# Kernel optimization log

Measured on AMD Instinct MI355X. Metric: run time of the kernel, lower is better.

Reference implementation:

```python
import jax, jax.numpy as jnp
import numpy as np

H_BLK, K_BLK = 2, 2      # h = out_ch//64, k = in_ch//64
HOS = 64                 # hyper_out_size
NR = 8                   # num_radii of hypernet-generated filters
KS = 3                   # kernel size
SD, HD = 6, 128          # seidel_dim, hyper_dim
CIN, COUT = K_BLK * HOS, H_BLK * HOS
B, HH, WW = 2, 256, 256
BN_EPS = 1e-5


def setup_inputs() -> dict:
    key = jax.random.key(0)
    ks = jax.random.split(key, 16)
    rn = lambda k, shape, s=1.0: jax.random.normal(k, shape, dtype=jnp.float32) * s
    n1, n2 = H_BLK * K_BLK, H_BLK * H_BLK
    hyper_out = HOS * HOS * NR * KS * KS  # 294912
    return {
        "x": rn(ks[0], (B, CIN, HH, WW)),
        "seidel": rn(ks[1], (B, SD)),
        "m1_w1": rn(ks[2], (n1, SD, HD), 1.0 / np.sqrt(SD)),
        "m1_b1": rn(ks[3], (n1, HD), 0.01),
        "m1_w2": rn(ks[4], (n1, HD, HD), 1.0 / np.sqrt(HD)),
        "m1_b2": rn(ks[5], (n1, HD), 0.01),
        "m2_w1": rn(ks[6], (n2, SD, HD), 1.0 / np.sqrt(SD)),
        "m2_b1": rn(ks[7], (n2, HD), 0.01),
        "m2_w2": rn(ks[8], (n2, HD, HD), 1.0 / np.sqrt(HD)),
        "m2_b2": rn(ks[9], (n2, HD), 0.01),
        "hyper_w": rn(ks[10], (HD, hyper_out), 0.02),
        "hyper_b": rn(ks[11], (hyper_out,), 0.01),
        "bn1_gamma": jnp.ones((COUT,), jnp.float32),
        "bn1_beta": jnp.zeros((COUT,), jnp.float32),
        "bn2_gamma": jnp.ones((COUT,), jnp.float32),
        "bn2_beta": jnp.zeros((COUT,), jnp.float32),
    }


def _gen_weights(s, mw1, mb1, mw2, mb2, hyper_w, hyper_b, rows, cols):
    # s: [SD]; one MLP per (row, col) block, hypernet shared.
    e = jax.nn.relu(jnp.einsum('i,nio->no', s, mw1) + mb1)       # [n, HD]
    e = jax.nn.relu(jnp.einsum('ni,nio->no', e, mw2) + mb2)      # [n, HD] (dropout = eval identity)
    blk = (e @ hyper_w + hyper_b).reshape(rows, cols, HOS, HOS, NR, KS, KS)
    # cat dim=1 over cols (c_in), cat dim=0 over rows (c_out)
    return blk.transpose(0, 2, 1, 3, 4, 5, 6).reshape(rows * HOS, cols * HOS, NR, KS, KS)


def _interp_w(w, wd):
    # trilinear interp (align_corners=False) along radii axis to wd points; k,k axes are identity.
    nr = w.shape[2]
    pos = jnp.clip((jnp.arange(wd, dtype=jnp.float32) + 0.5) * (nr / wd) - 0.5, 0.0, nr - 1.0)
    i0 = jnp.floor(pos).astype(jnp.int32)
    i1 = jnp.minimum(i0 + 1, nr - 1)
    f = (pos - i0.astype(jnp.float32))[None, None, :, None, None]
    return w[:, :, i0] * (1.0 - f) + w[:, :, i1] * f              # [cout, cin, wd, KS, KS]


def _lri_conv(x1, wi):
    # x1: [cin, H, W]; wi: [cout, cin, W, KS, KS]; circular pad in H, zero pad in W.
    c, h, w = x1.shape
    p = 1
    xp = jnp.pad(x1, ((0, 0), (p, p), (0, 0)), mode='wrap')
    xp = jnp.pad(xp, ((0, 0), (0, 0), (p, p)))
    out = jnp.zeros((wi.shape[0], h, w), x1.dtype)
    for ki in range(KS):
        for kj in range(KS):
            out = out + jnp.einsum('ihw,oiw->ohw', xp[:, ki:ki + h, kj:kj + w], wi[:, :, :, ki, kj])
    return out


def _bn_relu(y, g, b):
    # per-item training-mode BN (torch loop feeds one item at a time): stats over H,W per channel
    mu = y.mean(axis=(1, 2), keepdims=True)
    var = y.var(axis=(1, 2), keepdims=True)
    return jax.nn.relu(g[:, None, None] * (y - mu) * jax.lax.rsqrt(var + BN_EPS) + b[:, None, None])


def _forward(x, seidel, m1_w1, m1_b1, m1_w2, m1_b2, m2_w1, m2_b1, m2_w2, m2_b2,
             hyper_w, hyper_b, bn1_gamma, bn1_beta, bn2_gamma, bn2_beta):
    wd = x.shape[-1]

    def per_item(xi, si):
        w1 = _interp_w(_gen_weights(si, m1_w1, m1_b1, m1_w2, m1_b2, hyper_w, hyper_b, H_BLK, K_BLK), wd)
        y = _bn_relu(_lri_conv(xi, w1), bn1_gamma, bn1_beta)
        w2 = _interp_w(_gen_weights(si, m2_w1, m2_b1, m2_w2, m2_b2, hyper_w, hyper_b, H_BLK, H_BLK), wd)
        return _bn_relu(_lri_conv(y, w2), bn2_gamma, bn2_beta)

    return jax.vmap(per_item)(x, seidel)


def reference(x, seidel, m1_w1, m1_b1, m1_w2, m1_b2, m2_w1, m2_b1, m2_w2, m2_b2,
              hyper_w, hyper_b, bn1_gamma, bn1_beta, bn2_gamma, bn2_beta):
    return _forward(x, seidel, m1_w1, m1_b1, m1_w2, m1_b2, m2_w1, m2_b1, m2_w2, m2_b2,
                    hyper_w, hyper_b, bn1_gamma, bn1_beta, bn2_gamma, bn2_beta)
```

## Files before the change

kernel.cpp:

```cpp
#include <hip/hip_runtime.h>
#include <hip/hip_bf16.h>


#define SD 6
#define HD 128
#define HYPER_OUT 294912
#define BN_EPS 1e-5f

typedef unsigned short ushort_t;
typedef __attribute__((ext_vector_type(8))) short bf16x8;
typedef __attribute__((ext_vector_type(4))) float f32x4;

__device__ inline ushort_t f2bf(float f) {
  union { float f; unsigned u; } v; v.f = f;
  unsigned r = v.u + 0x7fffu + ((v.u >> 16) & 1u);
  return (ushort_t)(r >> 16);
}
__device__ inline float bf2f(ushort_t h) {
  union { unsigned u; float f; } v; v.u = ((unsigned)h) << 16; return v.f;
}
__device__ inline unsigned pack2(float a, float b) {
  return (unsigned)f2bf(a) | ((unsigned)f2bf(b) << 16);
}

__device__ inline bf16x8 lerp8d(bf16x8 a, bf16x8 d, float f) {
  union U { bf16x8 v; unsigned u[4]; };
  U A, D, R;
  A.v = a; D.v = d;
  #pragma unroll
  for (int i = 0; i < 4; ++i) {
    float alo = __uint_as_float(A.u[i] << 16);
    float ahi = __uint_as_float(A.u[i] & 0xffff0000u);
    float dlo = __uint_as_float(D.u[i] << 16);
    float dhi = __uint_as_float(D.u[i] & 0xffff0000u);
    float rlo = fmaf(f, dlo, alo);
    float rhi = fmaf(f, dhi, ahi);
    __hip_bfloat162 h2 = __float22bfloat162_rn(float2{rlo, rhi});
    R.u[i] = *reinterpret_cast<unsigned*>(&h2);
  }
  return R.v;
}

__device__ inline int as_off(int row, int cu) {
  return row*128 + ((cu ^ (row & 7)) << 3);
}

__global__ __launch_bounds__(128) void k_mlp(
    const float* __restrict__ seidel,
    const float* __restrict__ m1_w1, const float* __restrict__ m1_b1,
    const float* __restrict__ m1_w2, const float* __restrict__ m1_b2,
    const float* __restrict__ m2_w1, const float* __restrict__ m2_b1,
    const float* __restrict__ m2_w2, const float* __restrict__ m2_b2,
    float* __restrict__ e_all)
{
  int b = blockIdx.x;
  int item = b >> 3, conv = (b >> 2) & 1, n = b & 3;
  const float* w1 = conv ? m2_w1 : m1_w1;
  const float* b1 = conv ? m2_b1 : m1_b1;
  const float* w2 = conv ? m2_w2 : m1_w2;
  const float* b2 = conv ? m2_b2 : m1_b2;
  int t = threadIdx.x;
  __shared__ float e1[HD];
  float s = b1[n*HD + t];
  #pragma unroll
  for (int i = 0; i < SD; ++i) s = fmaf(seidel[item*SD + i], w1[(n*SD + i)*HD + t], s);
  e1[t] = fmaxf(s, 0.f);
  __syncthreads();
  float s2 = b2[n*HD + t];
  for (int i = 0; i < HD; ++i) s2 = fmaf(e1[i], w2[(n*HD + i)*HD + t], s2);
  e_all[b*HD + t] = fmaxf(s2, 0.f);
}

__global__ __launch_bounds__(256) void k_hyper(
    const float* __restrict__ e_all, const float* __restrict__ hyper_w,
    const float* __restrict__ hyper_b, ushort_t* __restrict__ wb_lin)
{
  __shared__ float es[16*HD];
  int t = threadIdx.x;
  for (int f = t; f < 16*HD; f += 256) es[f] = e_all[f];
  __syncthreads();
  int j = blockIdx.x*256 + t;
  float val[16];
  #pragma unroll
  for (int r = 0; r < 16; ++r) val[r] = 0.f;
  for (int i = 0; i < HD; ++i) {
    float hw = hyper_w[(size_t)i*HYPER_OUT + j];
    #pragma unroll
    for (int r = 0; r < 16; ++r) val[r] = fmaf(es[r*HD + i], hw, val[r]);
  }
  float bias = hyper_b[j];
  uint4 u0, u1;
  u0.x = pack2(val[0]+bias,  val[1]+bias);
  u0.y = pack2(val[2]+bias,  val[3]+bias);
  u0.z = pack2(val[4]+bias,  val[5]+bias);
  u0.w = pack2(val[6]+bias,  val[7]+bias);
  u1.x = pack2(val[8]+bias,  val[9]+bias);
  u1.y = pack2(val[10]+bias, val[11]+bias);
  u1.z = pack2(val[12]+bias, val[13]+bias);
  u1.w = pack2(val[14]+bias, val[15]+bias);
  *reinterpret_cast<uint4*>(wb_lin + (size_t)j*16)     = u0;
  *reinterpret_cast<uint4*>(wb_lin + (size_t)j*16 + 8) = u1;
}

__global__ __launch_bounds__(256) void k_prep(
    const float* __restrict__ x, ushort_t* __restrict__ xt,
    const ushort_t* __restrict__ wb_lin,
    ushort_t* __restrict__ wbW, ushort_t* __restrict__ wbD)
{
  __shared__ __align__(16) float tileF[64][65];
  __shared__ ushort_t ldsN[16][256];
  int b = blockIdx.x;
  int t = threadIdx.x;
  if (b < 4096) {
    int wt = b & 3, ct = (b >> 2) & 1, z = b >> 3;
    int h = z & 255, item = z >> 8;
    {
      int cl = t >> 2, wk = (t & 3) << 4;
      const float* sp = x + (((size_t)item*128 + ct*64 + cl)*256 + h)*256 + wt*64 + wk;
      #pragma unroll
      for (int k = 0; k < 16; k += 4) {
        float4 v = *reinterpret_cast<const float4*>(sp + k);
        tileF[cl][wk+k] = v.x; tileF[cl][wk+k+1] = v.y;
        tileF[cl][wk+k+2] = v.z; tileF[cl][wk+k+3] = v.w;
      }
    }
    __syncthreads();
    {
      int wl = t >> 2, ck = (t & 3) << 4;
      ushort_t* dp = xt + (((size_t)item*256 + wt*64 + wl)*256 + h)*128 + ct*64 + ck;
      uint4 u0, u1;
      u0.x = pack2(tileF[ck+0][wl],  tileF[ck+1][wl]);
      u0.y = pack2(tileF[ck+2][wl],  tileF[ck+3][wl]);
      u0.z = pack2(tileF[ck+4][wl],  tileF[ck+5][wl]);
      u0.w = pack2(tileF[ck+6][wl],  tileF[ck+7][wl]);
      u1.x = pack2(tileF[ck+8][wl],  tileF[ck+9][wl]);
      u1.y = pack2(tileF[ck+10][wl], tileF[ck+11][wl]);
      u1.z = pack2(tileF[ck+12][wl], tileF[ck+13][wl]);
      u1.w = pack2(tileF[ck+14][wl], tileF[ck+15][wl]);
      *reinterpret_cast<uint4*>(dp)     = u0;
      *reinterpret_cast<uint4*>(dp + 8) = u1;
    }
  } else {
    int i = b - 4096;
    int chunk = i & 15;
    int tap   = i >> 4;
    int nr = tap / 9, kk = tap % 9;
    int ki = kk / 3, kj = kk % 3;
    int nrn = (nr < 7) ? nr + 1 : 7;
    ushort_t (*lds)[256] = reinterpret_cast<ushort_t(*)[256]>(tileF);
    int uv = chunk*256 + t;
    size_t j  = (size_t)uv*72 + nr*9 + kk;
    size_t j2 = (size_t)uv*72 + nrn*9 + kk;
    uint4 q0 = *reinterpret_cast<const uint4*>(wb_lin + j*16);
    uint4 q1 = *reinterpret_cast<const uint4*>(wb_lin + j*16 + 8);
    uint4 n0 = *reinterpret_cast<const uint4*>(wb_lin + j2*16);
    uint4 n1 = *reinterpret_cast<const uint4*>(wb_lin + j2*16 + 8);
    const ushort_t* pr0 = reinterpret_cast<const ushort_t*>(&q0);
    const ushort_t* pr1 = reinterpret_cast<const ushort_t*>(&q1);
    const ushort_t* pn0 = reinterpret_cast<const ushort_t*>(&n0);
    const ushort_t* pn1 = reinterpret_cast<const ushort_t*>(&n1);
    #pragma unroll
    for (int r = 0; r < 8; ++r) { lds[r][t]  = pr0[r]; ldsN[r][t]  = pn0[r]; }
    #pragma unroll
    for (int r = 0; r < 8; ++r) { lds[r+8][t] = pr1[r]; ldsN[r+8][t] = pn1[r]; }
    __syncthreads();
    #pragma unroll
    for (int it = 0; it < 2; ++it) {
      int idx = it*256 + t;
      int row = idx >> 3, seg = idx & 7;
      int p = row >> 2, ul = row & 3;
      int item = p >> 3, conv = (p >> 2) & 1, n = p & 3;
      int o  = (n >> 1)*64 + chunk*4 + ul;
      int c8 = (n & 1)*8 + seg;
      int ch = c8 >> 2, gq = c8 & 3;
      int oblk = o >> 4, ol = o & 15;
      uint4 v = *reinterpret_cast<const uint4*>(&lds[p][ul*64 + seg*8]);
      uint4 d4;
      {
        const ushort_t* pw = reinterpret_cast<const ushort_t*>(&v);
        const ushort_t* pnx = &ldsN[p][ul*64 + seg*8];
        ushort_t* pd = reinterpret_cast<ushort_t*>(&d4);
        #pragma unroll
        for (int e = 0; e < 8; ++e) pd[e] = f2bf(bf2f(pnx[e]) - bf2f(pw[e]));
      }
      size_t off = (size_t)(conv*2 + item)*1179648
                 + ((((size_t)nr*3 + kj)*3 + ki)*4 + ch)*4096
                 + oblk*512 + (gq*16 + ol)*8;
      *reinterpret_cast<uint4*>(wbW + off) = v;
      *reinterpret_cast<uint4*>(wbD + off) = d4;
    }
  }
}

template<bool BN_IN>
__global__ __launch_bounds__(256, 2) void k_conv(
    const ushort_t* __restrict__ src,
    const ushort_t* __restrict__ wbW, const ushort_t* __restrict__ wbD,
    const float* __restrict__ bn_a, const float* __restrict__ bn_c,
    ushort_t* __restrict__ dst, float* __restrict__ ps, float* __restrict__ p2)
{
  __shared__ __align__(16) ushort_t As[258*128];
  __shared__ float sbn[256];
  int bid = blockIdx.x;
  int wgid = ((bid & 7) << 6) | (bid >> 3);
  int item = wgid >> 8;
  int w    = wgid & 255;
  int t = threadIdx.x;
  int lane = t & 63, wid = t >> 6;
  int l15 = lane & 15, g = lane >> 4;

  float pos = fminf(fmaxf((w + 0.5f)*0.03125f - 0.5f, 0.f), 7.f);
  int i0 = (int)pos; float fr = pos - (float)i0;

  if constexpr (BN_IN) {
    sbn[t] = (t < 128) ? bn_a[item*128 + t] : bn_c[item*128 + (t - 128)];
    __syncthreads();
  }

  const ushort_t* wpW = wbW + (size_t)item*1179648 + (size_t)i0*147456
                      + (wid*2)*512 + lane*8;
  const ushort_t* wpD = wbD + (size_t)item*1179648 + (size_t)i0*147456
                      + (wid*2)*512 + lane*8;

  f32x4 acc[2][16];
  #pragma unroll
  for (int a = 0; a < 2; ++a)
    #pragma unroll
    for (int b = 0; b < 16; ++b)
      acc[a][b] = (f32x4){0.f, 0.f, 0.f, 0.f};

  auto stage_as = [&](int kj) {
    int wc = w + kj - 1;
    bool valid = (wc >= 0) && (wc < 256);
    const ushort_t* sb = src + ((size_t)item*256 + (valid ? wc : 0))*32768;
    for (int f = t; f < 258*16; f += 256) {
      int row = f >> 4, cu = f & 15;
      uint4 v = make_uint4(0u, 0u, 0u, 0u);
      if (valid) {
        int hg = (row + 255) & 255;
        v = *reinterpret_cast<const uint4*>(sb + ((size_t)hg << 7) + (cu << 3));
        if constexpr (BN_IN) {
          ushort_t* pv = reinterpret_cast<ushort_t*>(&v);
          int c0 = cu << 3;
          #pragma unroll
          for (int jj = 0; jj < 8; ++jj) {
            float xv = bf2f(pv[jj]);
            xv = fmaxf(fmaf(sbn[c0 + jj], xv, sbn[128 + c0 + jj]), 0.f);
            pv[jj] = f2bf(xv);
          }
        }
      }
      *reinterpret_cast<uint4*>(&As[as_off(row, cu)]) = v;
    }
  };

  auto loadraw = [&](bf16x8* rw, bf16x8* rd, int s) {
    size_t so = (size_t)s*4096;
    #pragma unroll
    for (int mf = 0; mf < 2; ++mf) {
      rw[mf] = *reinterpret_cast<const bf16x8*>(wpW + so + mf*512);
      rd[mf] = *reinterpret_cast<const bf16x8*>(wpD + so + mf*512);
    }
  };

  bf16x8 rwA[2], rdA[2], rwB[2], rdB[2], lw[2];
  loadraw(rwA, rdA, 0);

  for (int kj = 0; kj < 3; ++kj) {
    __syncthreads();
    stage_as(kj);
    __syncthreads();
    #pragma unroll
    for (int s2 = 0; s2 < 12; ++s2) {
      int ki = s2 >> 2, ch = s2 & 3;
      int s = kj*12 + s2;
      bf16x8* cw = (s2 & 1) ? rwB : rwA;
      bf16x8* cd = (s2 & 1) ? rdB : rdA;
      bf16x8* nw = (s2 & 1) ? rwA : rwB;
      bf16x8* nd = (s2 & 1) ? rdA : rdB;
      loadraw(nw, nd, (s + 1 < 36) ? (s + 1) : 35);
      #pragma unroll
      for (int mf = 0; mf < 2; ++mf) lw[mf] = lerp8d(cw[mf], cd[mf], fr);
      #pragma unroll
      for (int pass = 0; pass < 4; ++pass) {
        bf16x8 bfr[4];
        #pragma unroll
        for (int q = 0; q < 4; ++q) {
          int nf = pass*4 + q;
          bfr[q] = *reinterpret_cast<const bf16x8*>(
              &As[as_off(nf*16 + l15 + ki, (ch << 2) + g)]);
        }
        #pragma unroll
        for (int mf = 0; mf < 2; ++mf)
          #pragma unroll
          for (int q = 0; q < 4; ++q)
            acc[mf][pass*4 + q] = __builtin_amdgcn_mfma_f32_16x16x32_bf16(
                lw[mf], bfr[q], acc[mf][pass*4 + q], 0, 0, 0);
      }
    }
  }

  ushort_t* yb = dst + ((size_t)item*256 + w)*32768;
  float ssum[2][4], s2sum[2][4];
  #pragma unroll
  for (int a = 0; a < 2; ++a)
    #pragma unroll
    for (int b = 0; b < 4; ++b) { ssum[a][b] = 0.f; s2sum[a][b] = 0.f; }
  #pragma unroll
  for (int mf = 0; mf < 2; ++mf) {
    #pragma unroll
    for (int nf = 0; nf < 16; ++nf) {
      float v[4];
      #pragma unroll
      for (int r4 = 0; r4 < 4; ++r4) {
        v[r4] = acc[mf][nf][r4];
        ssum[mf][r4] += v[r4];
        s2sum[mf][r4] = fmaf(v[r4], v[r4], s2sum[mf][r4]);
      }
      int h  = nf*16 + l15;
      int o0 = wid*32 + mf*16 + (g << 2);
      uint2 u; u.x = pack2(v[0], v[1]); u.y = pack2(v[2], v[3]);
      *reinterpret_cast<uint2*>(yb + (size_t)h*128 + o0) = u;
    }
  }
  #pragma unroll
  for (int mf = 0; mf < 2; ++mf)
    #pragma unroll
    for (int r4 = 0; r4 < 4; ++r4)
      #pragma unroll
      for (int m = 1; m < 16; m <<= 1) {
        ssum[mf][r4]  += __shfl_xor(ssum[mf][r4], m);
        s2sum[mf][r4] += __shfl_xor(s2sum[mf][r4], m);
      }
  __syncthreads();
  float* redS  = reinterpret_cast<float*>(As);
  float* redS2 = redS + 128;
  if (l15 == 0) {
    #pragma unroll
    for (int mf = 0; mf < 2; ++mf)
      #pragma unroll
      for (int r4 = 0; r4 < 4; ++r4) {
        int o = wid*32 + mf*16 + (g << 2) + r4;
        redS [o] = ssum[mf][r4];
        redS2[o] = s2sum[mf][r4];
      }
  }
  __syncthreads();
  if (t < 128) {
    size_t bi = (size_t)item*256 + w;
    ps[bi*128 + t] = redS[t];
    p2[bi*128 + t] = redS2[t];
  }
}

__global__ __launch_bounds__(256) void k_bnapply(
    const float* __restrict__ ps, const float* __restrict__ p2,
    const float* __restrict__ gamma, const float* __restrict__ beta,
    float* __restrict__ bn_a, float* __restrict__ bn_c)
{
  int item = blockIdx.x >> 7, o = blockIdx.x & 127;
  int t = threadIdx.x;
  size_t bi = (size_t)(item*256 + t)*128 + o;
  float s  = ps[bi];
  float s2 = p2[bi];
  #pragma unroll
  for (int m = 1; m < 64; m <<= 1) { s += __shfl_xor(s, m); s2 += __shfl_xor(s2, m); }
  __shared__ float rs[4], rs2[4];
  if ((t & 63) == 0) { rs[t >> 6] = s; rs2[t >> 6] = s2; }
  __syncthreads();
  if (t == 0) {
    s  = rs[0] + rs[1] + rs[2] + rs[3];
    s2 = rs2[0] + rs2[1] + rs2[2] + rs2[3];
    float mu  = s  * (1.f/65536.f);
    float var = s2 * (1.f/65536.f) - mu*mu;
    float a = gamma[o] * rsqrtf(var + BN_EPS);
    bn_a[item*128 + o] = a;
    bn_c[item*128 + o] = beta[o] - a*mu;
  }
}

__global__ __launch_bounds__(256) void k_final(
    const ushort_t* __restrict__ y, const float* __restrict__ bn_a,
    const float* __restrict__ bn_c, float* __restrict__ out)
{
  __shared__ float tile[64][65];
  int wt = blockIdx.x, ot = blockIdx.y;
  int h = blockIdx.z & 255, item = blockIdx.z >> 8;
  int t = threadIdx.x;
  {
    int wl = t >> 2, ck = (t & 3) << 4;
    const ushort_t* sp = y + (((size_t)item*256 + wt*64 + wl)*256 + h)*128 + ot*64 + ck;
    uint4 a = *reinterpret_cast<const uint4*>(sp);
    uint4 b = *reinterpret_cast<const uint4*>(sp + 8);
    const ushort_t* pa = reinterpret_cast<const ushort_t*>(&a);
    const ushort_t* pb = reinterpret_cast<const ushort_t*>(&b);
    #pragma unroll
    for (int k = 0; k < 8; ++k) {
      int o = ot*64 + ck + k;
      tile[wl][ck + k] = fmaxf(fmaf(bn_a[item*128 + o], bf2f(pa[k]), bn_c[item*128 + o]), 0.f);
    }
    #pragma unroll
    for (int k = 0; k < 8; ++k) {
      int o = ot*64 + ck + 8 + k;
      tile[wl][ck + 8 + k] = fmaxf(fmaf(bn_a[item*128 + o], bf2f(pb[k]), bn_c[item*128 + o]), 0.f);
    }
  }
  __syncthreads();
  {
    int ol = t >> 2, wk = (t & 3) << 4;
    float* dp = out + (((size_t)item*128 + ot*64 + ol)*256 + h)*256 + wt*64 + wk;
    #pragma unroll
    for (int k = 0; k < 16; k += 4) {
      float4 v;
      v.x = tile[wk+k][ol];   v.y = tile[wk+k+1][ol];
      v.z = tile[wk+k+2][ol]; v.w = tile[wk+k+3][ol];
      *reinterpret_cast<float4*>(dp + k) = v;
    }
  }
}

extern "C" void kernel_launch(void* const* d_in, const int* in_sizes, int n_in,
                              void* d_out, int out_size, void* d_ws, size_t ws_size,
                              hipStream_t stream) {
  const float* x       = (const float*)d_in[0];
  const float* seidel  = (const float*)d_in[1];
  const float* m1_w1   = (const float*)d_in[2];
  const float* m1_b1   = (const float*)d_in[3];
  const float* m1_w2   = (const float*)d_in[4];
  const float* m1_b2   = (const float*)d_in[5];
  const float* m2_w1   = (const float*)d_in[6];
  const float* m2_b1   = (const float*)d_in[7];
  const float* m2_w2   = (const float*)d_in[8];
  const float* m2_b2   = (const float*)d_in[9];
  const float* hyper_w = (const float*)d_in[10];
  const float* hyper_b = (const float*)d_in[11];
  const float* bn1_g   = (const float*)d_in[12];
  const float* bn1_b   = (const float*)d_in[13];
  const float* bn2_g   = (const float*)d_in[14];
  const float* bn2_b   = (const float*)d_in[15];

  char* ws = (char*)d_ws;
  float*    e_all  = (float*)ws;
  ushort_t* wb_lin = (ushort_t*)(ws + 8192);
  ushort_t* wbW    = (ushort_t*)(ws + 9445376);
  ushort_t* wbD    = (ushort_t*)(ws + 18882560);
  ushort_t* xt     = (ushort_t*)(ws + 28319744);
  ushort_t* y1     = (ushort_t*)(ws + 61874176);
  ushort_t* y2     = (ushort_t*)(ws + 95428608);
  float*    ps     = (float*)(ws + 128983040);
  float*    p2     = (float*)(ws + 129245184);
  float*    bnb    = (float*)(ws + 129507328);
  float* bn1_a = bnb,        *bn1_c = bnb + 256;
  float* bn2_a = bnb + 512,  *bn2_c = bnb + 768;

  k_mlp<<<16, 128, 0, stream>>>(seidel, m1_w1, m1_b1, m1_w2, m1_b2,
                                m2_w1, m2_b1, m2_w2, m2_b2, e_all);
  k_hyper<<<HYPER_OUT/256, 256, 0, stream>>>(e_all, hyper_w, hyper_b, wb_lin);
  k_prep<<<5248, 256, 0, stream>>>(x, xt, wb_lin, wbW, wbD);

  k_conv<false><<<512, 256, 0, stream>>>(xt, wbW, wbD, nullptr, nullptr, y1, ps, p2);
  k_bnapply<<<256, 256, 0, stream>>>(ps, p2, bn1_g, bn1_b, bn1_a, bn1_c);

  k_conv<true><<<512, 256, 0, stream>>>(y1, wbW + 2359296, wbD + 2359296,
                                        bn1_a, bn1_c, y2, ps, p2);
  k_bnapply<<<256, 256, 0, stream>>>(ps, p2, bn2_g, bn2_b, bn2_a, bn2_c);
  k_final<<<dim3(4, 2, 512), 256, 0, stream>>>(y2, bn2_a, bn2_c, (float*)d_out);
}
```

Measured before the change: 256.9 us.

## Switch conv inner product to 32x32x16 MFMA with matching weight layout

The conv kernel moves from 16x16x32 bf16 MFMA tiles (2x16 fragments per wave) to 32x32x16 tiles (8 fragments of 32 outputs by 32 rows). The weight pre-pack kernel is rewritten to emit the matching per-lane layout. Each K-slice now needs one weight fragment and one lerp per lane instead of two, and each A-fragment LDS read feeds a larger MFMA. This is meant to cut LDS traffic and lerp work per FLOP. In exchange there are twice as many K steps, and the reduction shuffles and the epilogue output mapping change.

```diff
diff --git a/kernel.cpp b/kernel.cpp
--- a/kernel.cpp
+++ b/kernel.cpp
@@ -8,8 +8,8 @@
 #define BN_EPS 1e-5f
 
 typedef unsigned short ushort_t;
-typedef __attribute__((ext_vector_type(8))) short bf16x8;
-typedef __attribute__((ext_vector_type(4))) float f32x4;
+typedef __attribute__((ext_vector_type(8)))  short bf16x8;
+typedef __attribute__((ext_vector_type(16))) float f32x16;
 
 __device__ inline ushort_t f2bf(float f) {
   union { float f; unsigned u; } v; v.f = f;
@@ -172,8 +172,9 @@
       int item = p >> 3, conv = (p >> 2) & 1, n = p & 3;
       int o  = (n >> 1)*64 + chunk*4 + ul;
       int c8 = (n & 1)*8 + seg;
-      int ch = c8 >> 2, gq = c8 & 3;
-      int oblk = o >> 4, ol = o & 15;
+      int slice = ki*8 + (c8 >> 1);
+      int lane  = (o & 31) + (c8 & 1)*32;
+      int oblk  = o >> 5;
       uint4 v = *reinterpret_cast<const uint4*>(&lds[p][ul*64 + seg*8]);
       uint4 d4;
       {
@@ -184,8 +185,7 @@
         for (int e = 0; e < 8; ++e) pd[e] = f2bf(bf2f(pnx[e]) - bf2f(pw[e]));
       }
       size_t off = (size_t)(conv*2 + item)*1179648
-                 + ((((size_t)nr*3 + kj)*3 + ki)*4 + ch)*4096
-                 + oblk*512 + (gq*16 + ol)*8;
+                 + ((((size_t)nr*3 + kj)*24 + slice)*4 + oblk)*512 + lane*8;
       *reinterpret_cast<uint4*>(wbW + off) = v;
       *reinterpret_cast<uint4*>(wbD + off) = d4;
     }
@@ -207,7 +207,7 @@
   int w    = wgid & 255;
   int t = threadIdx.x;
   int lane = t & 63, wid = t >> 6;
-  int l15 = lane & 15, g = lane >> 4;
+  int l31 = lane & 31, kh = lane >> 5;
 
   float pos = fminf(fmaxf((w + 0.5f)*0.03125f - 0.5f, 0.f), 7.f);
   int i0 = (int)pos; float fr = pos - (float)i0;
@@ -218,16 +218,16 @@
   }
 
   const ushort_t* wpW = wbW + (size_t)item*1179648 + (size_t)i0*147456
-                      + (wid*2)*512 + lane*8;
+                      + wid*512 + lane*8;
   const ushort_t* wpD = wbD + (size_t)item*1179648 + (size_t)i0*147456
-                      + (wid*2)*512 + lane*8;
-
-  f32x4 acc[2][16];
-  #pragma unroll
-  for (int a = 0; a < 2; ++a)
+                      + wid*512 + lane*8;
+
+  f32x16 acc[8];
+  #pragma unroll
+  for (int a = 0; a < 8; ++a)
     #pragma unroll
     for (int b = 0; b < 16; ++b)
-      acc[a][b] = (f32x4){0.f, 0.f, 0.f, 0.f};
+      acc[a][b] = 0.f;
 
   auto stage_as = [&](int kj) {
     int wc = w + kj - 1;
@@ -254,95 +254,83 @@
     }
   };
 
-  auto loadraw = [&](bf16x8* rw, bf16x8* rd, int s) {
-    size_t so = (size_t)s*4096;
-    #pragma unroll
-    for (int mf = 0; mf < 2; ++mf) {
-      rw[mf] = *reinterpret_cast<const bf16x8*>(wpW + so + mf*512);
-      rd[mf] = *reinterpret_cast<const bf16x8*>(wpD + so + mf*512);
-    }
-  };
-
-  bf16x8 rwA[2], rdA[2], rwB[2], rdB[2], lw[2];
-  loadraw(rwA, rdA, 0);
+  bf16x8 rwA, rdA, rwB, rdB, lw;
+  rwA = *reinterpret_cast<const bf16x8*>(wpW);
+  rdA = *reinterpret_cast<const bf16x8*>(wpD);
 
   for (int kj = 0; kj < 3; ++kj) {
     __syncthreads();
     stage_as(kj);
     __syncthreads();
     #pragma unroll
-    for (int s2 = 0; s2 < 12; ++s2) {
-      int ki = s2 >> 2, ch = s2 & 3;
-      int s = kj*12 + s2;
-      bf16x8* cw = (s2 & 1) ? rwB : rwA;
-      bf16x8* cd = (s2 & 1) ? rdB : rdA;
-      bf16x8* nw = (s2 & 1) ? rwA : rwB;
-      bf16x8* nd = (s2 & 1) ? rdA : rdB;
-      loadraw(nw, nd, (s + 1 < 36) ? (s + 1) : 35);
-      #pragma unroll
-      for (int mf = 0; mf < 2; ++mf) lw[mf] = lerp8d(cw[mf], cd[mf], fr);
-      #pragma unroll
-      for (int pass = 0; pass < 4; ++pass) {
-        bf16x8 bfr[4];
-        #pragma unroll
-        for (int q = 0; q < 4; ++q) {
-          int nf = pass*4 + q;
-          bfr[q] = *reinterpret_cast<const bf16x8*>(
-              &As[as_off(nf*16 + l15 + ki, (ch << 2) + g)]);
-        }
-        #pragma unroll
-        for (int mf = 0; mf < 2; ++mf)
-          #pragma unroll
-          for (int q = 0; q < 4; ++q)
-            acc[mf][pass*4 + q] = __builtin_amdgcn_mfma_f32_16x16x32_bf16(
-                lw[mf], bfr[q], acc[mf][pass*4 + q], 0, 0, 0);
-      }
+    for (int sl = 0; sl < 24; ++sl) {
+      int ki = sl >> 3, c16 = sl & 7;
+      int s = kj*24 + sl;
+      size_t nxt = (size_t)((s + 1 < 72) ? s + 1 : 71)*2048;
+      if ((sl & 1) == 0) {
+        rwB = *reinterpret_cast<const bf16x8*>(wpW + nxt);
+        rdB = *reinterpret_cast<const bf16x8*>(wpD + nxt);
+        lw = lerp8d(rwA, rdA, fr);
+      } else {
+        rwA = *reinterpret_cast<const bf16x8*>(wpW + nxt);
+        rdA = *reinterpret_cast<const bf16x8*>(wpD + nxt);
+        lw = lerp8d(rwB, rdB, fr);
+      }
+      bf16x8 bfr[8];
+      #pragma unroll
+      for (int nt = 0; nt < 8; ++nt)
+        bfr[nt] = *reinterpret_cast<const bf16x8*>(
+            &As[as_off(nt*32 + l31 + ki, c16*2 + kh)]);
+      #pragma unroll
+      for (int nt = 0; nt < 8; ++nt)
+        acc[nt] = __builtin_amdgcn_mfma_f32_32x32x16_bf16(
+            lw, bfr[nt], acc[nt], 0, 0, 0);
     }
   }
 
   ushort_t* yb = dst + ((size_t)item*256 + w)*32768;
-  float ssum[2][4], s2sum[2][4];
-  #pragma unroll
-  for (int a = 0; a < 2; ++a)
+  float ssum[4][4], s2sum[4][4];
+  #pragma unroll
+  for (int a = 0; a < 4; ++a)
     #pragma unroll
     for (int b = 0; b < 4; ++b) { ssum[a][b] = 0.f; s2sum[a][b] = 0.f; }
   #pragma unroll
-  for (int mf = 0; mf < 2; ++mf) {
-    #pragma unroll
-    for (int nf = 0; nf < 16; ++nf) {
+  for (int nt = 0; nt < 8; ++nt) {
+    int h = nt*32 + l31;
+    #pragma unroll
+    for (int rq = 0; rq < 4; ++rq) {
       float v[4];
       #pragma unroll
       for (int r4 = 0; r4 < 4; ++r4) {
-        v[r4] = acc[mf][nf][r4];
-        ssum[mf][r4] += v[r4];
-        s2sum[mf][r4] = fmaf(v[r4], v[r4], s2sum[mf][r4]);
-      }
-      int h  = nf*16 + l15;
-      int o0 = wid*32 + mf*16 + (g << 2);
+        v[r4] = acc[nt][rq*4 + r4];
+        ssum[rq][r4] += v[r4];
+        s2sum[rq][r4] = fmaf(v[r4], v[r4], s2sum[rq][r4]);
+      }
+      int o0 = wid*32 + rq*8 + kh*4;
       uint2 u; u.x = pack2(v[0], v[1]); u.y = pack2(v[2], v[3]);
       *reinterpret_cast<uint2*>(yb + (size_t)h*128 + o0) = u;
     }
   }
   #pragma unroll
-  for (int mf = 0; mf < 2; ++mf)
+  for (int rq = 0; rq < 4; ++rq)
     #pragma unroll
     for (int r4 = 0; r4 < 4; ++r4)
       #pragma unroll
-      for (int m = 1; m < 16; m <<= 1) {
-        ssum[mf][r4]  += __shfl_xor(ssum[mf][r4], m);
-        s2sum[mf][r4] += __shfl_xor(s2sum[mf][r4], m);
+      for (int m = 1; m < 32; m <<= 1) {
+        ssum[rq][r4]  += __shfl_xor(ssum[rq][r4], m);
+        s2sum[rq][r4] += __shfl_xor(s2sum[rq][r4], m);
       }
   __syncthreads();
   float* redS  = reinterpret_cast<float*>(As);
   float* redS2 = redS + 128;
-  if (l15 == 0) {
-    #pragma unroll
-    for (int mf = 0; mf < 2; ++mf)
+  if (l31 == 0) {
+    #pragma unroll
+    for (int rq = 0; rq < 4; ++rq)
       #pragma unroll
       for (int r4 = 0; r4 < 4; ++r4) {
-        int o = wid*32 + mf*16 + (g << 2) + r4;
-        redS [o] = ssum[mf][r4];
-        redS2[o] = s2sum[mf][r4];
+        int o = wid*32 + rq*8 + kh*4 + r4;
+        redS [o] = ssum[rq][r4];
+        redS2[o] = s2sum[rq][r4];
       }
   }
   __syncthreads();
```

Result: slower. 270.5 us (+5.3%).
